# Kernel tuning notes

Measured on AMD Instinct MI355X. Metric: run time of the kernel, lower is better.

Reference implementation:

```python
import jax, jax.numpy as jnp
import numpy as np

B, S, I, H = 64, 512, 512, 1024


def setup_inputs() -> dict:
    key = jax.random.key(0)
    ks = jax.random.split(key, 5)
    bound = 1.0 / np.sqrt(H)  # nn.GRUCell default init
    u = lambda k, shape: jax.random.uniform(k, shape, jnp.float32, -bound, bound)
    return {
        "input": jax.random.normal(ks[0], (B, S, I), jnp.float32),
        "state": jnp.zeros((B, H), jnp.float32),
        "weight_ih": u(ks[1], (3 * H, I)),
        "weight_hh": u(ks[2], (3 * H, H)),
        "bias_ih": u(ks[3], (3 * H,)),
        "bias_hh": u(ks[4], (3 * H,)),
        "gamma_ih": jnp.ones((3 * H,), jnp.float32),
        "gamma_hh": jnp.ones((3 * H,), jnp.float32),
    }


def _ln_x(x, g, b):
    # kefirski's _layer_norm_x: (x - mean) / std (unbiased std, eps=0)
    mean = jnp.mean(x, axis=-1, keepdims=True)
    std = jnp.std(x, axis=-1, keepdims=True, ddof=1)
    return g * ((x - mean) / std) + b


def _ln_h(x, g, b):
    # kefirski's _layer_norm_h: mean-subtraction only
    return g * (x - jnp.mean(x, axis=-1, keepdims=True)) + b


def reference(input, state, weight_ih, weight_hh, bias_ih, bias_hh, gamma_ih, gamma_hh):
    Hd = state.shape[-1]
    # Input-side projections + LN are h-independent -> precompute over all timesteps
    ih = jnp.einsum("bsi,gi->bsg", input, weight_ih)  # [B,S,3H]
    ih_rz = _ln_x(ih[..., : 2 * Hd], gamma_ih[: 2 * Hd], bias_ih[: 2 * Hd])  # [B,S,2H]
    ih_n = _ln_x(ih[..., 2 * Hd :], gamma_ih[2 * Hd :], bias_ih[2 * Hd :])  # [B,S,H]

    def step(h, xs):
        irz, inn = xs  # [B,2H], [B,H]
        hh = h @ weight_hh.T  # [B,3H]
        hh_rz = _ln_h(hh[:, : 2 * Hd], gamma_hh[: 2 * Hd], bias_hh[: 2 * Hd])
        hh_n = _ln_h(hh[:, 2 * Hd :], gamma_hh[2 * Hd :], bias_hh[2 * Hd :])
        rz = jax.nn.sigmoid(irz + hh_rz)
        r, z = rz[:, :Hd], rz[:, Hd:]
        n = jnp.tanh(inn + r * hh_n)
        h_new = (1.0 - z) * n + z * h
        return h_new, h_new

    final_state, outs = jax.lax.scan(
        step, state, (ih_rz.transpose(1, 0, 2), ih_n.transpose(1, 0, 2))
    )
    return outs.transpose(1, 0, 2), final_state  # [B,S,H], [B,H]
```

## Files before the change

### kernel.cpp

```cpp
#include <hip/hip_runtime.h>
#include <stdint.h>
#include <stddef.h>

#define B_  64
#define S_  512
#define I_  512
#define H_  1024
#define G_  3072
#define NWG 64
#define CPW 32

typedef short short8 __attribute__((ext_vector_type(8)));
typedef float f32x4  __attribute__((ext_vector_type(4)));
typedef unsigned short u16x4 __attribute__((ext_vector_type(4)));

__device__ __forceinline__ unsigned short f32_to_bf16(float f){
  unsigned u = __builtin_bit_cast(unsigned, f);
  u = (u + 0x7FFFu + ((u >> 16) & 1u)) >> 16;
  return (unsigned short)u;
}
__device__ __forceinline__ float bf16_to_f32(unsigned short s){
  unsigned u = ((unsigned)s) << 16;
  return __builtin_bit_cast(float, u);
}
__device__ __forceinline__ float sig_(float x){ return 1.0f/(1.0f + __expf(-x)); }
__device__ __forceinline__ float tanh_(float x){
  float ax = fabsf(x);
  float t = __expf(-2.0f*ax);
  float r = (1.0f - t)/(1.0f + t);
  return copysignf(r, x);
}

__device__ __forceinline__ short8 ldg16_coh(const unsigned short* p){
  short8 r;
  asm volatile("global_load_dwordx4 %0, %1, off sc0 sc1" : "=v"(r) : "v"(p) : "memory");
  return r;
}
__device__ __forceinline__ void stg8_coh(unsigned short* p, u16x4 v){
  asm volatile("global_store_dwordx2 %0, %1, off sc0 sc1" :: "v"(p), "v"(v) : "memory");
}
__device__ __forceinline__ void stg4_coh(unsigned* p, unsigned v){
  asm volatile("global_store_dword %0, %1, off sc0 sc1" :: "v"(p), "v"(v) : "memory");
}
__device__ __forceinline__ unsigned ldg4_coh(const unsigned* p){
  unsigned r;
  asm volatile("global_load_dword %0, %1, off sc0 sc1" : "=v"(r) : "v"(p) : "memory");
  return r;
}
__device__ __forceinline__ u16x4 ldg8(const unsigned short* p){
  u16x4 r;
  asm volatile("global_load_dwordx2 %0, %1, off" : "=v"(r) : "v"(p) : "memory");
  return r;
}

__global__ __launch_bounds__(256) void k_cvt4(const float* __restrict__ src,
                                              unsigned short* __restrict__ dst, int n4){
  int i = blockIdx.x*blockDim.x + threadIdx.x;
  int st = gridDim.x*blockDim.x;
  for (; i < n4; i += st){
    f32x4 v = *(const f32x4*)(src + (size_t)i*4);
    u16x4 o;
    o[0]=f32_to_bf16(v[0]); o[1]=f32_to_bf16(v[1]);
    o[2]=f32_to_bf16(v[2]); o[3]=f32_to_bf16(v[3]);
    *(u16x4*)(dst + (size_t)i*4) = o;
  }
}

__global__ __launch_bounds__(256) void k_cmean(const float* __restrict__ whh,
                                               unsigned short* __restrict__ CM){
  int k = blockIdx.x*256 + threadIdx.x;
  float s0 = 0.f, s1 = 0.f;
  for (int j = 0; j < 2048; ++j) s0 += whh[(size_t)j*H_ + k];
  for (int j = 2048; j < 3072; ++j) s1 += whh[(size_t)j*H_ + k];
  CM[k]      = f32_to_bf16(s0 * (1.0f/2048.0f));
  CM[H_ + k] = f32_to_bf16(s1 * (1.0f/1024.0f));
  for (int r = 2; r < 16; ++r) CM[(size_t)r*H_ + k] = 0;
}

__global__ __launch_bounds__(256, 2) void k_gemm_ih(
    const unsigned short* __restrict__ X,
    const unsigned short* __restrict__ W,
    unsigned short* __restrict__ IH,
    float* __restrict__ STAT)
{
  __shared__ __align__(16) short As[128*32];
  __shared__ __align__(16) short Bs[128*32];
  int bid = blockIdx.x;
  int mt = bid / 24, nt = bid % 24;
  int tid = threadIdx.x, lane = tid & 63, wid = tid >> 6;
  int vr = wid >> 1, vc = wid & 1;
  int r0s = tid >> 2, r1s = r0s + 64;
  int sc = (tid & 3) * 8;
  const unsigned short* xa0 = X + (size_t)(mt*128 + r0s)*512 + sc;
  const unsigned short* xa1 = X + (size_t)(mt*128 + r1s)*512 + sc;
  const unsigned short* wb0 = W + (size_t)(nt*128 + r0s)*512 + sc;
  const unsigned short* wb1 = W + (size_t)(nt*128 + r1s)*512 + sc;

  f32x4 acc[4][4];
  #pragma unroll
  for (int m=0;m<4;m++)
    #pragma unroll
    for (int n=0;n<4;n++) acc[m][n] = (f32x4){0.f,0.f,0.f,0.f};

  short8 ra0 = *(const short8*)xa0;
  short8 ra1 = *(const short8*)xa1;
  short8 rb0 = *(const short8*)wb0;
  short8 rb1 = *(const short8*)wb1;
  int ko = (lane >> 4) * 8;

  for (int kt = 0; kt < 16; ++kt){
    __syncthreads();
    *(short8*)&As[r0s*32 + sc] = ra0;
    *(short8*)&As[r1s*32 + sc] = ra1;
    *(short8*)&Bs[r0s*32 + sc] = rb0;
    *(short8*)&Bs[r1s*32 + sc] = rb1;
    __syncthreads();
    if (kt < 15){
      ra0 = *(const short8*)(xa0 + (kt+1)*32);
      ra1 = *(const short8*)(xa1 + (kt+1)*32);
      rb0 = *(const short8*)(wb0 + (kt+1)*32);
      rb1 = *(const short8*)(wb1 + (kt+1)*32);
    }
    short8 af[4], bfr[4];
    #pragma unroll
    for (int m=0;m<4;m++) af[m]  = *(const short8*)&As[(vr*64 + m*16 + (lane&15))*32 + ko];
    #pragma unroll
    for (int n=0;n<4;n++) bfr[n] = *(const short8*)&Bs[(vc*64 + n*16 + (lane&15))*32 + ko];
    #pragma unroll
    for (int m=0;m<4;m++)
      #pragma unroll
      for (int n=0;n<4;n++)
        acc[m][n] = __builtin_amdgcn_mfma_f32_16x16x32_bf16(af[m], bfr[n], acc[m][n], 0,0,0);
  }
  int row0 = mt*128 + vr*64, col0 = nt*128 + vc*64;
  int rl = (lane >> 4) * 4, cl = lane & 15;
  #pragma unroll
  for (int m=0;m<4;m++)
    #pragma unroll
    for (int n=0;n<4;n++)
      #pragma unroll
      for (int r=0;r<4;r++){
        int row = row0 + m*16 + rl + r;
        int rowT = ((row & 511) << 6) | (row >> 9);
        IH[(size_t)rowT*G_ + (col0 + n*16 + cl)] = f32_to_bf16(acc[m][n][r]);
      }

  const int soff = (nt < 16) ? 0 : 2;
  #pragma unroll
  for (int m=0;m<4;m++)
    #pragma unroll
    for (int r=0;r<4;r++){
      float s1 = 0.f, s2 = 0.f;
      #pragma unroll
      for (int n=0;n<4;n++){ float v = acc[m][n][r]; s1 += v; s2 += v*v; }
      #pragma unroll
      for (int off=1; off<16; off<<=1){
        s1 += __shfl_xor(s1, off, 16);
        s2 += __shfl_xor(s2, off, 16);
      }
      if (cl == 0){
        int row = row0 + m*16 + rl + r;
        float* sp = STAT + (size_t)row*4 + soff;
        atomicAdd(sp,     s1);
        atomicAdd(sp + 1, s2);
      }
    }
}

__global__ __launch_bounds__(256, 1) void k_gru(
    const unsigned short* __restrict__ IH,
    const unsigned short* __restrict__ WHH,
    const unsigned short* __restrict__ CM,
    unsigned short* __restrict__ HB,
    const float* __restrict__ ghh,
    const float* __restrict__ bhh,
    const float* __restrict__ gih,
    const float* __restrict__ bih,
    const float* __restrict__ STAT,
    const float* __restrict__ state,
    float* __restrict__ out,
    unsigned* __restrict__ FLAGS)
{
  __shared__ float PSUM[4][112][34];
  const int g = blockIdx.x & 31;
  const int p = blockIdx.x >> 5;
  const int tid = threadIdx.x;
  const int lane = tid & 63;
  const int wv = tid >> 6;
  const int l15 = lane & 15;
  const int lho = (lane >> 4) << 3;
  const int colbase = g * CPW;
  const int rowbase = p * 32;

  short8 bfr[7][8];
  #pragma unroll
  for (int ct = 0; ct < 7; ++ct){
    const unsigned short* src = (ct < 6)
        ? (WHH + (size_t)((ct>>1)*H_ + colbase + (ct&1)*16 + l15)*H_)
        : (CM + (size_t)l15*H_);
    #pragma unroll
    for (int ks = 0; ks < 8; ++ks)
      bfr[ct][ks] = *(const short8*)(src + wv*256 + ks*32 + lho);
  }

  const int b_ = tid & 31;
  const int cq = tid >> 5;
  const int c0 = colbase + cq*4;
  const int gb = rowbase + b_;
  float gr[4],gz[4],gn[4],br_[4],bz_[4],bn_[4];
  float gir[4],giz[4],gin[4],bir[4],biz[4],bin[4],hv[4];
  #pragma unroll
  for (int j = 0; j < 4; ++j){
    int col = c0 + j;
    gr[j] = ghh[col];   gz[j] = ghh[H_+col];   gn[j] = ghh[2*H_+col];
    br_[j]= bhh[col];   bz_[j]= bhh[H_+col];   bn_[j]= bhh[2*H_+col];
    gir[j]= gih[col];   giz[j]= gih[H_+col];   gin[j]= gih[2*H_+col];
    bir[j]= bih[col];   biz[j]= bih[H_+col];   bin[j]= bih[2*H_+col];
    hv[j] = state[(size_t)gb*H_ + col];
  }

  const unsigned* fbase = FLAGS + (size_t)(p*32 + wv*8 + (lane & 7))*16;
  unsigned* pubflag = FLAGS + (size_t)(p*32 + g)*16;

  for (int t = 0; t < S_; ++t){
    const unsigned short* hbR = HB + (t & 1)*(B_*H_);
    unsigned short*       hbW = (unsigned short*)HB + ((t+1) & 1)*(B_*H_);

    const unsigned short* ihp = IH + ((size_t)t*B_ + gb)*G_;
    u16x4 ir  = ldg8(ihp + c0);
    u16x4 izv = ldg8(ihp + H_ + c0);
    u16x4 inv = ldg8(ihp + 2*H_ + c0);
    f32x4 sv = *(const f32x4*)(STAT + (((size_t)gb << 9) | t)*4);

    short8 af[8][2];
    unsigned pend = 0xFFu;
    do {
      unsigned v = ldg4_coh(fbase);
      asm volatile("s_waitcnt vmcnt(0)" ::: "memory");
      __builtin_amdgcn_sched_barrier(0);
      unsigned long long bl = __ballot((int)(v >= (unsigned)t));
      unsigned newly = ((unsigned)bl & 0xFFu) & pend;
      #pragma unroll
      for (int ks = 0; ks < 8; ++ks){
        if (newly & (1u << ks)){
          af[ks][0] = ldg16_coh(hbR + (size_t)(rowbase + l15)*H_      + wv*256 + ks*32 + lho);
          af[ks][1] = ldg16_coh(hbR + (size_t)(rowbase + 16 + l15)*H_ + wv*256 + ks*32 + lho);
        }
      }
      pend &= ~newly;
    } while (pend);
    asm volatile("s_waitcnt vmcnt(0)" ::: "memory");
    __builtin_amdgcn_sched_barrier(0);

    f32x4 acc[7][2];
    #pragma unroll
    for (int ct = 0; ct < 7; ++ct)
      #pragma unroll
      for (int rt = 0; rt < 2; ++rt)
        acc[ct][rt] = (f32x4){0.f,0.f,0.f,0.f};
    #pragma unroll
    for (int ks = 0; ks < 8; ++ks)
      #pragma unroll
      for (int rt = 0; rt < 2; ++rt)
        #pragma unroll
        for (int ct = 0; ct < 7; ++ct)
          acc[ct][rt] = __builtin_amdgcn_mfma_f32_16x16x32_bf16(af[ks][rt], bfr[ct][ks], acc[ct][rt], 0,0,0);

    #pragma unroll
    for (int ct = 0; ct < 7; ++ct)
      #pragma unroll
      for (int rt = 0; rt < 2; ++rt)
        *(f32x4*)&PSUM[wv][ct*16 + l15][rt*16 + (lane>>4)*4] = acc[ct][rt];
    __syncthreads();

    float hhr[4]={0,0,0,0}, hhz[4]={0,0,0,0}, hhn[4]={0,0,0,0};
    float mrz = 0.f, mn = 0.f;
    #pragma unroll
    for (int w = 0; w < 4; ++w){
      #pragma unroll
      for (int j = 0; j < 4; ++j){
        hhr[j] += PSUM[w][cq*4 + j][b_];
        hhz[j] += PSUM[w][32 + cq*4 + j][b_];
        hhn[j] += PSUM[w][64 + cq*4 + j][b_];
      }
      mrz += PSUM[w][96][b_];
      mn  += PSUM[w][97][b_];
    }
    float m0 = sv[0] * (1.0f/2048.0f);
    float rs0 = rsqrtf(fmaxf((sv[1] - sv[0]*m0) * (1.0f/2047.0f), 1e-20f));
    float m1 = sv[2] * (1.0f/1024.0f);
    float rs1 = rsqrtf(fmaxf((sv[3] - sv[2]*m1) * (1.0f/1023.0f), 1e-20f));
    f32x4 ho;
    u16x4 h16;
    #pragma unroll
    for (int j = 0; j < 4; ++j){
      float xr = gir[j]*(bf16_to_f32(ir[j])  - m0)*rs0 + bir[j];
      float xz = giz[j]*(bf16_to_f32(izv[j]) - m0)*rs0 + biz[j];
      float xn = gin[j]*(bf16_to_f32(inv[j]) - m1)*rs1 + bin[j];
      float R = sig_(xr + gr[j]*(hhr[j]-mrz) + br_[j]);
      float Z = sig_(xz + gz[j]*(hhz[j]-mrz) + bz_[j]);
      float N = tanh_(xn + R*(gn[j]*(hhn[j]-mn) + bn_[j]));
      hv[j] = (1.0f - Z)*N + Z*hv[j];
      ho[j] = hv[j];
      h16[j] = f32_to_bf16(hv[j]);
    }
    *(f32x4*)(out + ((size_t)gb*S_ + t)*H_ + c0) = ho;
    stg8_coh(hbW + (size_t)gb*H_ + c0, h16);

    asm volatile("s_waitcnt vmcnt(0)" ::: "memory");
    __syncthreads();
    if (tid == 0) stg4_coh(pubflag, (unsigned)(t+1));
  }
  #pragma unroll
  for (int j = 0; j < 4; ++j)
    out[(size_t)B_*S_*H_ + (size_t)gb*H_ + c0 + j] = hv[j];
}

extern "C" void kernel_launch(void* const* d_in, const int* in_sizes, int n_in,
                              void* d_out, int out_size, void* d_ws, size_t ws_size,
                              hipStream_t stream){
  (void)in_sizes; (void)n_in; (void)out_size; (void)ws_size;
  const float* x   = (const float*)d_in[0];
  const float* st  = (const float*)d_in[1];
  const float* wih = (const float*)d_in[2];
  const float* whh = (const float*)d_in[3];
  const float* bih = (const float*)d_in[4];
  const float* bhh = (const float*)d_in[5];
  const float* gih = (const float*)d_in[6];
  const float* ghh = (const float*)d_in[7];
  float* out = (float*)d_out;
  char* ws = (char*)d_ws;

  unsigned short* IH    = (unsigned short*)(ws);
  unsigned short* X16   = (unsigned short*)(ws + 201326592ull);
  unsigned short* WIH16 = (unsigned short*)(ws + 234881024ull);
  unsigned short* WHH16 = (unsigned short*)(ws + 238026752ull);
  unsigned short* CM16  = (unsigned short*)(ws + 244318208ull);
  unsigned short* HB    = (unsigned short*)(ws + 244350976ull);
  unsigned*       FLAGS = (unsigned*)      (ws + 244613120ull);
  float*          STAT  = (float*)         (ws + 244617216ull);

  hipMemsetAsync(FLAGS, 0, 4096, stream);
  hipMemsetAsync(STAT, 0, 524288, stream);
  k_cvt4<<<2048, 256, 0, stream>>>(x,   X16,   4194304);
  k_cvt4<<<1024, 256, 0, stream>>>(wih, WIH16, 393216);
  k_cvt4<<<1024, 256, 0, stream>>>(whh, WHH16, 786432);
  k_cvt4<<<64,   256, 0, stream>>>(st,  HB,    16384);
  k_cmean<<<4,   256, 0, stream>>>(whh, CM16);
  k_gemm_ih<<<6144, 256, 0, stream>>>(X16, WIH16, IH, STAT);
  k_gru<<<NWG, 256, 0, stream>>>(IH, WHH16, CM16, HB, ghh, bhh, gih, bih, STAT, st, out, FLAGS);
}
```

Before: 3.710 ms.

## Halve GRU workgroups to 32 with 512 threads and simplify flag wait

```diff
diff --git a/kernel.cpp b/kernel.cpp
--- a/kernel.cpp
+++ b/kernel.cpp
@@ -7,8 +7,8 @@
 #define I_  512
 #define H_  1024
 #define G_  3072
-#define NWG 64
-#define CPW 32
+#define NWG 32
+#define CPW 64
 
 typedef short short8 __attribute__((ext_vector_type(8)));
 typedef float f32x4  __attribute__((ext_vector_type(4)));
@@ -42,9 +42,10 @@
 __device__ __forceinline__ void stg4_coh(unsigned* p, unsigned v){
   asm volatile("global_store_dword %0, %1, off sc0 sc1" :: "v"(p), "v"(v) : "memory");
 }
-__device__ __forceinline__ unsigned ldg4_coh(const unsigned* p){
+__device__ __forceinline__ unsigned ldg4_coh_wait(const unsigned* p){
   unsigned r;
-  asm volatile("global_load_dword %0, %1, off sc0 sc1" : "=v"(r) : "v"(p) : "memory");
+  asm volatile("global_load_dword %0, %1, off sc0 sc1\n\ts_waitcnt vmcnt(0)"
+               : "=v"(r) : "v"(p) : "memory");
   return r;
 }
 __device__ __forceinline__ u16x4 ldg8(const unsigned short* p){
@@ -167,7 +168,7 @@
     }
 }
 
-__global__ __launch_bounds__(256, 1) void k_gru(
+__global__ __launch_bounds__(512, 1) void k_gru(
     const unsigned short* __restrict__ IH,
     const unsigned short* __restrict__ WHH,
     const unsigned short* __restrict__ CM,
@@ -181,46 +182,45 @@
     float* __restrict__ out,
     unsigned* __restrict__ FLAGS)
 {
-  __shared__ float PSUM[4][112][34];
-  const int g = blockIdx.x & 31;
-  const int p = blockIdx.x >> 5;
+  __shared__ float PSUM[2][4][112][34];
+  const int strip = blockIdx.x & 15;
+  const int p = blockIdx.x >> 4;
   const int tid = threadIdx.x;
   const int lane = tid & 63;
   const int wv = tid >> 6;
+  const int kq = wv & 3;
+  const int cp = wv >> 2;
   const int l15 = lane & 15;
   const int lho = (lane >> 4) << 3;
-  const int colbase = g * CPW;
+  const int colbase = strip * CPW;
   const int rowbase = p * 32;
 
   short8 bfr[7][8];
   #pragma unroll
   for (int ct = 0; ct < 7; ++ct){
     const unsigned short* src = (ct < 6)
-        ? (WHH + (size_t)((ct>>1)*H_ + colbase + (ct&1)*16 + l15)*H_)
+        ? (WHH + (size_t)((ct>>1)*H_ + colbase + cp*32 + (ct&1)*16 + l15)*H_)
         : (CM + (size_t)l15*H_);
     #pragma unroll
     for (int ks = 0; ks < 8; ++ks)
-      bfr[ct][ks] = *(const short8*)(src + wv*256 + ks*32 + lho);
+      bfr[ct][ks] = *(const short8*)(src + kq*256 + ks*32 + lho);
   }
 
   const int b_ = tid & 31;
   const int cq = tid >> 5;
   const int c0 = colbase + cq*4;
   const int gb = rowbase + b_;
-  float gr[4],gz[4],gn[4],br_[4],bz_[4],bn_[4];
-  float gir[4],giz[4],gin[4],bir[4],biz[4],bin[4],hv[4];
+  float gr[4],gz[4],gn[4],br_[4],bz_[4],bn_[4],hv[4];
   #pragma unroll
   for (int j = 0; j < 4; ++j){
     int col = c0 + j;
     gr[j] = ghh[col];   gz[j] = ghh[H_+col];   gn[j] = ghh[2*H_+col];
     br_[j]= bhh[col];   bz_[j]= bhh[H_+col];   bn_[j]= bhh[2*H_+col];
-    gir[j]= gih[col];   giz[j]= gih[H_+col];   gin[j]= gih[2*H_+col];
-    bir[j]= bih[col];   biz[j]= bih[H_+col];   bin[j]= bih[2*H_+col];
     hv[j] = state[(size_t)gb*H_ + col];
   }
 
-  const unsigned* fbase = FLAGS + (size_t)(p*32 + wv*8 + (lane & 7))*16;
-  unsigned* pubflag = FLAGS + (size_t)(p*32 + g)*16;
+  const unsigned* myflag = FLAGS + (size_t)(p*16 + (lane & 15))*16;
+  unsigned* pubflag = FLAGS + (size_t)(p*16 + strip)*16;
 
   for (int t = 0; t < S_; ++t){
     const unsigned short* hbR = HB + (t & 1)*(B_*H_);
@@ -230,25 +230,25 @@
     u16x4 ir  = ldg8(ihp + c0);
     u16x4 izv = ldg8(ihp + H_ + c0);
     u16x4 inv = ldg8(ihp + 2*H_ + c0);
-    f32x4 sv = *(const f32x4*)(STAT + (((size_t)gb << 9) | t)*4);
+    f32x4 sv  = *(const f32x4*)(STAT + (((size_t)gb << 9) | (size_t)t)*4);
+    f32x4 lgr = *(const f32x4*)(gih + c0);
+    f32x4 lgz = *(const f32x4*)(gih + H_ + c0);
+    f32x4 lgn = *(const f32x4*)(gih + 2*H_ + c0);
+    f32x4 lbr = *(const f32x4*)(bih + c0);
+    f32x4 lbz = *(const f32x4*)(bih + H_ + c0);
+    f32x4 lbn = *(const f32x4*)(bih + 2*H_ + c0);
+
+    for (;;){
+      unsigned v = ldg4_coh_wait(myflag);
+      if (__all((int)(v >= (unsigned)t))) break;
+    }
 
     short8 af[8][2];
-    unsigned pend = 0xFFu;
-    do {
-      unsigned v = ldg4_coh(fbase);
-      asm volatile("s_waitcnt vmcnt(0)" ::: "memory");
-      __builtin_amdgcn_sched_barrier(0);
-      unsigned long long bl = __ballot((int)(v >= (unsigned)t));
-      unsigned newly = ((unsigned)bl & 0xFFu) & pend;
-      #pragma unroll
-      for (int ks = 0; ks < 8; ++ks){
-        if (newly & (1u << ks)){
-          af[ks][0] = ldg16_coh(hbR + (size_t)(rowbase + l15)*H_      + wv*256 + ks*32 + lho);
-          af[ks][1] = ldg16_coh(hbR + (size_t)(rowbase + 16 + l15)*H_ + wv*256 + ks*32 + lho);
-        }
-      }
-      pend &= ~newly;
-    } while (pend);
+    #pragma unroll
+    for (int ks = 0; ks < 8; ++ks)
+      #pragma unroll
+      for (int rt = 0; rt < 2; ++rt)
+        af[ks][rt] = ldg16_coh(hbR + (size_t)(rowbase + rt*16 + l15)*H_ + kq*256 + ks*32 + lho);
     asm volatile("s_waitcnt vmcnt(0)" ::: "memory");
     __builtin_amdgcn_sched_barrier(0);
 
@@ -270,21 +270,23 @@
     for (int ct = 0; ct < 7; ++ct)
       #pragma unroll
       for (int rt = 0; rt < 2; ++rt)
-        *(f32x4*)&PSUM[wv][ct*16 + l15][rt*16 + (lane>>4)*4] = acc[ct][rt];
+        *(f32x4*)&PSUM[cp][kq][ct*16 + l15][rt*16 + (lane>>4)*4] = acc[ct][rt];
     __syncthreads();
 
+    const int ch = cq >> 3;
+    const int cc = (cq & 7) * 4;
     float hhr[4]={0,0,0,0}, hhz[4]={0,0,0,0}, hhn[4]={0,0,0,0};
     float mrz = 0.f, mn = 0.f;
     #pragma unroll
     for (int w = 0; w < 4; ++w){
       #pragma unroll
       for (int j = 0; j < 4; ++j){
-        hhr[j] += PSUM[w][cq*4 + j][b_];
-        hhz[j] += PSUM[w][32 + cq*4 + j][b_];
-        hhn[j] += PSUM[w][64 + cq*4 + j][b_];
+        hhr[j] += PSUM[ch][w][cc + j][b_];
+        hhz[j] += PSUM[ch][w][32 + cc + j][b_];
+        hhn[j] += PSUM[ch][w][64 + cc + j][b_];
       }
-      mrz += PSUM[w][96][b_];
-      mn  += PSUM[w][97][b_];
+      mrz += PSUM[0][w][96][b_];
+      mn  += PSUM[0][w][97][b_];
     }
     float m0 = sv[0] * (1.0f/2048.0f);
     float rs0 = rsqrtf(fmaxf((sv[1] - sv[0]*m0) * (1.0f/2047.0f), 1e-20f));
@@ -294,9 +296,9 @@
     u16x4 h16;
     #pragma unroll
     for (int j = 0; j < 4; ++j){
-      float xr = gir[j]*(bf16_to_f32(ir[j])  - m0)*rs0 + bir[j];
-      float xz = giz[j]*(bf16_to_f32(izv[j]) - m0)*rs0 + biz[j];
-      float xn = gin[j]*(bf16_to_f32(inv[j]) - m1)*rs1 + bin[j];
+      float xr = lgr[j]*(bf16_to_f32(ir[j])  - m0)*rs0 + lbr[j];
+      float xz = lgz[j]*(bf16_to_f32(izv[j]) - m0)*rs0 + lbz[j];
+      float xn = lgn[j]*(bf16_to_f32(inv[j]) - m1)*rs1 + lbn[j];
       float R = sig_(xr + gr[j]*(hhr[j]-mrz) + br_[j]);
       float Z = sig_(xz + gz[j]*(hhz[j]-mrz) + bz_[j]);
       float N = tanh_(xn + R*(gn[j]*(hhn[j]-mn) + bn_[j]));
@@ -348,5 +350,5 @@
   k_cvt4<<<64,   256, 0, stream>>>(st,  HB,    16384);
   k_cmean<<<4,   256, 0, stream>>>(whh, CM16);
   k_gemm_ih<<<6144, 256, 0, stream>>>(X16, WIH16, IH, STAT);
-  k_gru<<<NWG, 256, 0, stream>>>(IH, WHH16, CM16, HB, ghh, bhh, gih, bih, STAT, st, out, FLAGS);
-}
+  k_gru<<<NWG, 512, 0, stream>>>(IH, WHH16, CM16, HB, ghh, bhh, gih, bih, STAT, st, out, FLAGS);
+}
```

Result: slower. 10.78 ms (+190.4%).
